# Performance work log

Hardware: AMD Instinct MI355X
Metric: run time of the kernel (lower is better)

Reference implementation:

```python
import jax, jax.numpy as jnp
import numpy as np

LAMB = 5.0
B, N = 1024, 3125  # batch, anchors (5 anchors x 25x25 map)

def setup_inputs() -> dict:
    key = jax.random.key(0)
    k1, k2, k3, k4 = jax.random.split(key, 4)
    return {
        "c_pred": jax.random.normal(k1, (B, N, 2), dtype=jnp.float32),
        "r_pred": jax.random.normal(k2, (B, N, 4), dtype=jnp.float32),
        "r_target": jax.random.normal(k3, (B, N, 4), dtype=jnp.float32),
        # anchor labels in {-1: ignore, 0: negative, 1: positive}
        "label": jax.random.randint(k4, (B, N), -1, 2, dtype=jnp.int32),
    }

def reference(c_pred, r_pred, r_target, label):
    dt = c_pred.dtype
    pos = (label == 1)
    neg = (label == 0)
    pos_cnt = pos.sum(axis=-1).astype(dt)  # [B]
    neg_cnt = neg.sum(axis=-1).astype(dt)

    # --- classification: masked 2-class cross-entropy, pos/neg balanced per batch ---
    logp = jax.nn.log_softmax(c_pred, axis=-1)  # [B, N, 2]
    ce_pos = -logp[..., 1]                      # CE when target class = 1
    ce_neg = -logp[..., 0]                      # CE when target class = 0
    pos_mean = jnp.where(pos_cnt > 0,
                         (ce_pos * pos).sum(axis=-1) / jnp.maximum(pos_cnt, 1.0), 0.0)
    neg_mean = (ce_neg * neg).sum(axis=-1) / jnp.maximum(neg_cnt, 1.0)
    c_loss = ((pos_mean + neg_mean) * 0.5).mean()

    d = r_pred - r_target
    a = jnp.abs(d)
    sl = jnp.where(a < 1.0, 0.5 * d * d, a - 0.5)  # [B, N, 4]
    # per-batch mean over pos_num*4 elements == masked mean of per-anchor coord-mean
    r_per = (sl.mean(axis=-1) * pos).sum(axis=-1) / jnp.maximum(pos_cnt, 1.0)
    r_loss = jnp.where(pos_cnt > 0, r_per, 0.0).mean()

    t_loss = c_loss + LAMB * r_loss
    return (c_loss, r_loss, t_loss)
```

## Files before the change

kernel.cpp:

```cpp
#include <hip/hip_runtime.h>

#define BATCH 1024
#define NANCH 3125
#define LAMB  5.0f
#define SPLIT 4
#define CHUNK ((NANCH + SPLIT - 1) / SPLIT)

__device__ __forceinline__ float wave_red_f(float v) {
    #pragma unroll
    for (int o = 32; o > 0; o >>= 1) v += __shfl_down(v, o, 64);
    return v;
}

__global__ __launch_bounds__(256) void partial_kernel(
    const float* __restrict__ c_pred,
    const float* __restrict__ r_pred,
    const float* __restrict__ r_target,
    const int*   __restrict__ label,
    float*       __restrict__ partial)
{
    const int blk = blockIdx.x;
    const int b   = blk / SPLIT;
    const int s   = blk % SPLIT;
    const int tid = threadIdx.x;

    const float2* c2 = (const float2*)(c_pred   + (size_t)b * NANCH * 2);
    const float4* rp = (const float4*)(r_pred   + (size_t)b * NANCH * 4);
    const float4* rt = (const float4*)(r_target + (size_t)b * NANCH * 4);
    const int*    lb = label + (size_t)b * NANCH;

    const int end = min((s + 1) * CHUNK, NANCH);

    float cp = 0.f, cn = 0.f, sl = 0.f, pc = 0.f, nc = 0.f;

    for (int i = s * CHUNK + tid; i < end; i += 256) {
        const int    l = lb[i];
        const float2 c = c2[i];
        const float4 p = rp[i];
        const float4 t = rt[i];

        const float isp = (l == 1) ? 1.f : 0.f;
        const float isn = (l == 0) ? 1.f : 0.f;

        const float m   = fmaxf(c.x, c.y);
        const float lse = m + log1pf(__expf(-fabsf(c.x - c.y)));

        pc += isp;
        nc += isn;
        cp += isp * (lse - c.y);
        cn += isn * (lse - c.x);

        float s4 = 0.f, d, a;
        d = p.x - t.x; a = fabsf(d); s4 += (a < 1.f) ? 0.5f * d * d : a - 0.5f;
        d = p.y - t.y; a = fabsf(d); s4 += (a < 1.f) ? 0.5f * d * d : a - 0.5f;
        d = p.z - t.z; a = fabsf(d); s4 += (a < 1.f) ? 0.5f * d * d : a - 0.5f;
        d = p.w - t.w; a = fabsf(d); s4 += (a < 1.f) ? 0.5f * d * d : a - 0.5f;
        sl += isp * s4 * 0.25f;
    }

    cp = wave_red_f(cp);
    cn = wave_red_f(cn);
    sl = wave_red_f(sl);
    pc = wave_red_f(pc);
    nc = wave_red_f(nc);

    __shared__ float sm[5][4];
    const int wid = tid >> 6, lane = tid & 63;
    if (lane == 0) {
        sm[0][wid] = cp; sm[1][wid] = cn; sm[2][wid] = sl;
        sm[3][wid] = pc; sm[4][wid] = nc;
    }
    __syncthreads();
    if (tid == 0) {
        float v0 = 0.f, v1 = 0.f, v2 = 0.f, v3 = 0.f, v4 = 0.f;
        #pragma unroll
        for (int w = 0; w < 4; ++w) {
            v0 += sm[0][w]; v1 += sm[1][w]; v2 += sm[2][w];
            v3 += sm[3][w]; v4 += sm[4][w];
        }
        float* o = partial + (size_t)blk * 5;
        o[0] = v0; o[1] = v1; o[2] = v2; o[3] = v3; o[4] = v4;
    }
}

__global__ __launch_bounds__(256) void finalize_kernel(
    const float* __restrict__ partial,
    float*       __restrict__ out)
{
    const int tid = threadIdx.x;
    float csum = 0.f, rsum = 0.f;

    for (int b = tid; b < BATCH; b += 256) {
        float cp = 0.f, cn = 0.f, sl = 0.f, pc = 0.f, nc = 0.f;
        #pragma unroll
        for (int s = 0; s < SPLIT; ++s) {
            const float* p = partial + ((size_t)b * SPLIT + s) * 5;
            cp += p[0]; cn += p[1]; sl += p[2]; pc += p[3]; nc += p[4];
        }
        const bool haspos = (pc > 0.5f);
        const float pos_mean = haspos ? cp / fmaxf(pc, 1.f) : 0.f;
        const float neg_mean = cn / fmaxf(nc, 1.f);
        csum += (pos_mean + neg_mean) * 0.5f;
        rsum += haspos ? sl / fmaxf(pc, 1.f) : 0.f;
    }

    csum = wave_red_f(csum);
    rsum = wave_red_f(rsum);

    __shared__ float s_c[4], s_r[4];
    const int wid = tid >> 6, lane = tid & 63;
    if (lane == 0) { s_c[wid] = csum; s_r[wid] = rsum; }
    __syncthreads();
    if (tid == 0) {
        float cs = 0.f, rs = 0.f;
        #pragma unroll
        for (int w = 0; w < 4; ++w) { cs += s_c[w]; rs += s_r[w]; }
        const float c_loss = cs / (float)BATCH;
        const float r_loss = rs / (float)BATCH;
        out[0] = c_loss;
        out[1] = r_loss;
        out[2] = c_loss + LAMB * r_loss;
    }
}

extern "C" void kernel_launch(void* const* d_in, const int* in_sizes, int n_in,
                              void* d_out, int out_size, void* d_ws, size_t ws_size,
                              hipStream_t stream) {
    const float* c_pred   = (const float*)d_in[0];
    const float* r_pred   = (const float*)d_in[1];
    const float* r_target = (const float*)d_in[2];
    const int*   label    = (const int*)d_in[3];
    float*       out      = (float*)d_out;
    float*       partial  = (float*)d_ws;

    partial_kernel<<<BATCH * SPLIT, 256, 0, stream>>>(c_pred, r_pred, r_target, label, partial);
    finalize_kernel<<<1, 256, 0, stream>>>(partial, out);
}
```

Measured before the change: 32.37 us.

## Fuse partial and finalize kernels via atomic accumulation with last-block finish

```diff
diff --git a/kernel.cpp b/kernel.cpp
--- a/kernel.cpp
+++ b/kernel.cpp
@@ -3,8 +3,7 @@
 #define BATCH 1024
 #define NANCH 3125
 #define LAMB  5.0f
-#define SPLIT 4
-#define CHUNK ((NANCH + SPLIT - 1) / SPLIT)
+#define INV_B (1.0f / 1024.0f)
 
 __device__ __forceinline__ float wave_red_f(float v) {
     #pragma unroll
@@ -12,16 +11,17 @@
     return v;
 }
 
-__global__ __launch_bounds__(256) void partial_kernel(
+__global__ __launch_bounds__(256) void fused_kernel(
     const float* __restrict__ c_pred,
     const float* __restrict__ r_pred,
     const float* __restrict__ r_target,
     const int*   __restrict__ label,
-    float*       __restrict__ partial)
+    float*       __restrict__ c_acc,
+    float*       __restrict__ r_acc,
+    unsigned*    __restrict__ counter,
+    float*       __restrict__ out)
 {
-    const int blk = blockIdx.x;
-    const int b   = blk / SPLIT;
-    const int s   = blk % SPLIT;
+    const int b   = blockIdx.x;
     const int tid = threadIdx.x;
 
     const float2* c2 = (const float2*)(c_pred   + (size_t)b * NANCH * 2);
@@ -29,11 +29,10 @@
     const float4* rt = (const float4*)(r_target + (size_t)b * NANCH * 4);
     const int*    lb = label + (size_t)b * NANCH;
 
-    const int end = min((s + 1) * CHUNK, NANCH);
-
     float cp = 0.f, cn = 0.f, sl = 0.f, pc = 0.f, nc = 0.f;
 
-    for (int i = s * CHUNK + tid; i < end; i += 256) {
+    #pragma unroll 2
+    for (int i = tid; i < NANCH; i += 256) {
         const int    l = lb[i];
         const float2 c = c2[i];
         const float4 p = rp[i];
@@ -43,7 +42,7 @@
         const float isn = (l == 0) ? 1.f : 0.f;
 
         const float m   = fmaxf(c.x, c.y);
-        const float lse = m + log1pf(__expf(-fabsf(c.x - c.y)));
+        const float lse = m + __logf(1.f + __expf(-fabsf(c.x - c.y)));
 
         pc += isp;
         nc += isn;
@@ -71,55 +70,30 @@
         sm[3][wid] = pc; sm[4][wid] = nc;
     }
     __syncthreads();
+
     if (tid == 0) {
-        float v0 = 0.f, v1 = 0.f, v2 = 0.f, v3 = 0.f, v4 = 0.f;
-        #pragma unroll
-        for (int w = 0; w < 4; ++w) {
-            v0 += sm[0][w]; v1 += sm[1][w]; v2 += sm[2][w];
-            v3 += sm[3][w]; v4 += sm[4][w];
+        const float tcp = sm[0][0] + sm[0][1] + sm[0][2] + sm[0][3];
+        const float tcn = sm[1][0] + sm[1][1] + sm[1][2] + sm[1][3];
+        const float tsl = sm[2][0] + sm[2][1] + sm[2][2] + sm[2][3];
+        const float tpc = sm[3][0] + sm[3][1] + sm[3][2] + sm[3][3];
+        const float tnc = sm[4][0] + sm[4][1] + sm[4][2] + sm[4][3];
+
+        const bool  haspos   = (tpc > 0.5f);
+        const float pos_mean = haspos ? tcp / tpc : 0.f;
+        const float neg_mean = tcn / fmaxf(tnc, 1.f);
+        const float c_contrib = (pos_mean + neg_mean) * 0.5f * INV_B;
+        const float r_contrib = (haspos ? tsl / tpc : 0.f) * INV_B;
+
+        __hip_atomic_fetch_add(c_acc, c_contrib, __ATOMIC_RELAXED, __HIP_MEMORY_SCOPE_AGENT);
+        __hip_atomic_fetch_add(r_acc, r_contrib, __ATOMIC_RELAXED, __HIP_MEMORY_SCOPE_AGENT);
+        const unsigned old = __hip_atomic_fetch_add(counter, 1u, __ATOMIC_ACQ_REL, __HIP_MEMORY_SCOPE_AGENT);
+        if (old == BATCH - 1) {
+            const float c_loss = __hip_atomic_load(c_acc, __ATOMIC_ACQUIRE, __HIP_MEMORY_SCOPE_AGENT);
+            const float r_loss = __hip_atomic_load(r_acc, __ATOMIC_ACQUIRE, __HIP_MEMORY_SCOPE_AGENT);
+            out[0] = c_loss;
+            out[1] = r_loss;
+            out[2] = c_loss + LAMB * r_loss;
         }
-        float* o = partial + (size_t)blk * 5;
-        o[0] = v0; o[1] = v1; o[2] = v2; o[3] = v3; o[4] = v4;
-    }
-}
-
-__global__ __launch_bounds__(256) void finalize_kernel(
-    const float* __restrict__ partial,
-    float*       __restrict__ out)
-{
-    const int tid = threadIdx.x;
-    float csum = 0.f, rsum = 0.f;
-
-    for (int b = tid; b < BATCH; b += 256) {
-        float cp = 0.f, cn = 0.f, sl = 0.f, pc = 0.f, nc = 0.f;
-        #pragma unroll
-        for (int s = 0; s < SPLIT; ++s) {
-            const float* p = partial + ((size_t)b * SPLIT + s) * 5;
-            cp += p[0]; cn += p[1]; sl += p[2]; pc += p[3]; nc += p[4];
-        }
-        const bool haspos = (pc > 0.5f);
-        const float pos_mean = haspos ? cp / fmaxf(pc, 1.f) : 0.f;
-        const float neg_mean = cn / fmaxf(nc, 1.f);
-        csum += (pos_mean + neg_mean) * 0.5f;
-        rsum += haspos ? sl / fmaxf(pc, 1.f) : 0.f;
-    }
-
-    csum = wave_red_f(csum);
-    rsum = wave_red_f(rsum);
-
-    __shared__ float s_c[4], s_r[4];
-    const int wid = tid >> 6, lane = tid & 63;
-    if (lane == 0) { s_c[wid] = csum; s_r[wid] = rsum; }
-    __syncthreads();
-    if (tid == 0) {
-        float cs = 0.f, rs = 0.f;
-        #pragma unroll
-        for (int w = 0; w < 4; ++w) { cs += s_c[w]; rs += s_r[w]; }
-        const float c_loss = cs / (float)BATCH;
-        const float r_loss = rs / (float)BATCH;
-        out[0] = c_loss;
-        out[1] = r_loss;
-        out[2] = c_loss + LAMB * r_loss;
     }
 }
 
@@ -131,8 +105,12 @@
     const float* r_target = (const float*)d_in[2];
     const int*   label    = (const int*)d_in[3];
     float*       out      = (float*)d_out;
-    float*       partial  = (float*)d_ws;
 
-    partial_kernel<<<BATCH * SPLIT, 256, 0, stream>>>(c_pred, r_pred, r_target, label, partial);
-    finalize_kernel<<<1, 256, 0, stream>>>(partial, out);
+    float*    c_acc   = (float*)d_ws;
+    float*    r_acc   = (float*)((char*)d_ws + 256);
+    unsigned* counter = (unsigned*)((char*)d_ws + 512);
+
+    hipMemsetAsync(d_ws, 0, 768, stream);
+    fused_kernel<<<BATCH, 256, 0, stream>>>(c_pred, r_pred, r_target, label,
+                                            c_acc, r_acc, counter, out);
 }
```

New measurement: 62.12 us. 1.92x slower.
